# Optimization experiments

Measured on AMD Instinct MI355X. Metric: run time of the kernel, lower is better.

## Reference

```python
import jax, jax.numpy as jnp
import numpy as np

MULT = 20.0 / 2 ** (5 - 2)  # level=2, num_levels=5, div_flow=20 -> 2.5
PATCH = 7
PAD = PATCH // 2


def up_flow_fn(flow, w):
    # ConvTranspose2d(2, 2, 4, stride=2, padding=1, groups=2, bias=False)
    wf = w[:, :, ::-1, ::-1]  # flip kernel -> equivalent dilated conv
    return jax.lax.conv_general_dilated(
        flow, wf, window_strides=(1, 1), padding=((2, 2), (2, 2)),
        lhs_dilation=(2, 2), dimension_numbers=('NCHW', 'OIHW', 'NCHW'),
        feature_group_count=2)


def warp(x, flow, mult):
    # ptlflow LiteFlowNet WarpingLayer: normalized grid + flow/div_flow, grid_sample
    # (border padding, align_corners=True) masked by zero-padded ones-sample >= 1.
    B, C, H, W = x.shape
    gx = jnp.linspace(-1.0, 1.0, W, dtype=x.dtype)[None, None, :]
    gy = jnp.linspace(-1.0, 1.0, H, dtype=x.dtype)[None, :, None]
    sx = gx + flow[:, 0] * (2.0 * mult / max(W - 1, 1))
    sy = gy + flow[:, 1] * (2.0 * mult / max(H - 1, 1))
    px = (sx + 1.0) * 0.5 * (W - 1)  # unnormalized coords, align_corners=True
    py = (sy + 1.0) * 0.5 * (H - 1)
    # --- border-padded bilinear sample of x ---
    pxc = jnp.clip(px, 0.0, W - 1.0)
    pyc = jnp.clip(py, 0.0, H - 1.0)
    x0 = jnp.floor(pxc); y0 = jnp.floor(pyc)
    tx = pxc - x0; ty = pyc - y0
    x0i = x0.astype(jnp.int32); y0i = y0.astype(jnp.int32)
    x1i = jnp.minimum(x0i + 1, W - 1); y1i = jnp.minimum(y0i + 1, H - 1)
    img = jnp.transpose(x, (0, 2, 3, 1))  # BHWC for gathers
    b = jnp.arange(B)[:, None, None]
    v00 = img[b, y0i, x0i]; v01 = img[b, y0i, x1i]
    v10 = img[b, y1i, x0i]; v11 = img[b, y1i, x1i]
    out = (v00 * ((1 - tx) * (1 - ty))[..., None] + v01 * (tx * (1 - ty))[..., None]
           + v10 * ((1 - tx) * ty)[..., None] + v11 * (tx * ty)[..., None])
    # --- zero-padded bilinear sample of ones -> validity mask ---
    fx0 = jnp.floor(px); fy0 = jnp.floor(py)
    mtx = px - fx0; mty = py - fy0
    m = jnp.zeros_like(px)
    for dy, dx, wgt in ((0, 0, (1 - mtx) * (1 - mty)), (0, 1, mtx * (1 - mty)),
                        (1, 0, (1 - mtx) * mty), (1, 1, mtx * mty)):
        xi = fx0 + dx; yi = fy0 + dy
        inb = (xi >= 0) & (xi <= W - 1) & (yi >= 0) & (yi <= H - 1)
        m = m + wgt * inb.astype(x.dtype)
    mask = (m >= 1.0).astype(x.dtype)[..., None]
    return jnp.transpose(out * mask, (0, 3, 1, 2))


def correlation(f1, f2):
    # SpatialCorrelationSampler(kernel_size=1, patch_size=7, stride=1, dilation_patch=1)
    # corr[b,d,i,j] = sum_c f1[b,c,i,j] * f2[b,c,i+di-3,j+dj-3] (zero pad), d = 7*di+dj
    B, C, H, W = f1.shape
    f2p = jnp.pad(f2, ((0, 0), (0, 0), (PAD, PAD), (PAD, PAD)))
    outs = [jnp.sum(f1 * f2p[:, :, di:di + H, dj:dj + W], axis=1)
            for di in range(PATCH) for dj in range(PATCH)]
    return jnp.stack(outs, axis=1)  # [B, 49, H, W]


def conv2d(x, w, b, pad):
    y = jax.lax.conv_general_dilated(
        x, w, window_strides=(1, 1), padding=((pad, pad), (pad, pad)),
        dimension_numbers=('NCHW', 'OIHW', 'NCHW'))
    return y + b[None, :, None, None]


def setup_inputs() -> dict:
    key = jax.random.key(0)
    ks = jax.random.split(key, 11)
    B, C, H, W = 4, 128, 192, 320
    feats = jax.random.normal(ks[0], (B, 2, C, H, W), jnp.float32)
    flow = jax.random.normal(ks[1], (B, 2, H // 2, W // 2), jnp.float32)
    up_w = jax.random.normal(ks[2], (2, 1, 4, 4), jnp.float32) * 0.25
    w1 = jax.random.normal(ks[3], (128, 49, 3, 3), jnp.float32) * 0.05
    b1 = jnp.zeros((128,), jnp.float32)
    w2 = jax.random.normal(ks[4], (64, 128, 3, 3), jnp.float32) * 0.03
    b2 = jnp.zeros((64,), jnp.float32)
    w3 = jax.random.normal(ks[5], (32, 64, 3, 3), jnp.float32) * 0.04
    b3 = jnp.zeros((32,), jnp.float32)
    w4 = jax.random.normal(ks[6], (2, 32, 5, 5), jnp.float32) * 0.03
    b4 = jnp.zeros((2,), jnp.float32)
    return {"feats": feats, "flow": flow, "up_w": up_w, "w1": w1, "b1": b1,
            "w2": w2, "b2": b2, "w3": w3, "b3": b3, "w4": w4, "b4": b4}


def reference(feats, flow, up_w, w1, b1, w2, b2, w3, b3, w4, b4):
    C = feats.shape[2]
    flow_up = up_flow_fn(flow, up_w)                    # [B,2,H,W]
    warped2 = warp(feats[:, 1], flow_up, MULT)          # warp feat2 by flow*mult
    corr = correlation(feats[:, 0], warped2)            # [B,49,H,W]
    corr = jax.nn.leaky_relu(corr, 0.1) / C
    h = jax.nn.leaky_relu(conv2d(corr, w1, b1, 1), 0.1)
    h = jax.nn.leaky_relu(conv2d(h, w2, b2, 1), 0.1)
    h = jax.nn.leaky_relu(conv2d(h, w3, b3, 1), 0.1)
    new_flow = conv2d(h, w4, b4, 2)                     # flow_kernel_size=5, pad=2
    return flow_up + new_flow
```

## Files before the change

kernel.cpp:

```cpp
#include <hip/hip_runtime.h>

typedef __attribute__((ext_vector_type(8))) short short8;
typedef __attribute__((ext_vector_type(4))) float f32x4;
typedef __attribute__((ext_vector_type(16))) float f32x16;
typedef unsigned int uint;

constexpr int B = 4, C = 128, H = 192, W = 320;
constexpr int HW_ = H * W;

__device__ __forceinline__ unsigned short f2bf(float x) {
    uint u = __float_as_uint(x);
    u += 0x7fffu + ((u >> 16) & 1u);
    return (unsigned short)(u >> 16);
}
__device__ __forceinline__ uint pack2bf(float a, float b) {
    return (uint)f2bf(a) | ((uint)f2bf(b) << 16);
}

__global__ __launch_bounds__(256) void upflow_kernel(
    const float* __restrict__ flow, const float* __restrict__ up_w,
    double* __restrict__ flow_up)
{
#pragma clang fp contract(off)
    int idx = blockIdx.x * 256 + threadIdx.x;
    if (idx >= B * 2 * HW_) return;
    int x = idx % W;
    int y = (idx / W) % H;
    int c = (idx / HW_) % 2;
    int b = idx / (2 * HW_);
    double acc = 0.0;
    #pragma unroll
    for (int ky = 0; ky < 4; ++ky) {
        int p = y + ky - 2;
        if (p < 0 || (p & 1) || (p >> 1) >= 96) continue;
        #pragma unroll
        for (int kx = 0; kx < 4; ++kx) {
            int q = x + kx - 2;
            if (q < 0 || (q & 1) || (q >> 1) >= 160) continue;
            double fv = (double)flow[((b * 2 + c) * 96 + (p >> 1)) * 160 + (q >> 1)];
            double wv = (double)up_w[c * 16 + (3 - ky) * 4 + (3 - kx)];
            double prod = fv * wv;
            acc = acc + prod;
        }
    }
    flow_up[idx] = acc;
}

__global__ __launch_bounds__(256) void warp_kernel(
    const float* __restrict__ feats, const double* __restrict__ flow_up,
    uint* __restrict__ wp)
{
#pragma clang fp contract(off)
    int raw = blockIdx.x;
    int eb  = (raw & 7) * 240 + (raw >> 3);
    int g = eb / 960;
    int idx = (eb % 960) * 256 + threadIdx.x;
    int x = idx % W;
    int y = (idx / W) % H;
    int b = idx / HW_;

    double f0 = flow_up[(size_t)(b * 2 + 0) * HW_ + y * W + x];
    double f1 = flow_up[(size_t)(b * 2 + 1) * HW_ + y * W + x];

    double stepx = 2.0 / (double)(W - 1);
    double stepy = 2.0 / (double)(H - 1);
    double gx = (x == W - 1) ? 1.0 : ((double)x * stepx + (-1.0));
    double gy = (y == H - 1) ? 1.0 : ((double)y * stepy + (-1.0));
    double cxs = 2.0 * 2.5 / (double)(W - 1);
    double cys = 2.0 * 2.5 / (double)(H - 1);
    double sx = gx + f0 * cxs;
    double sy = gy + f1 * cys;
    double px = (sx + 1.0) * 0.5 * (double)(W - 1);
    double py = (sy + 1.0) * 0.5 * (double)(H - 1);

    double pxc = px < 0.0 ? 0.0 : (px > (double)(W - 1) ? (double)(W - 1) : px);
    double pyc = py < 0.0 ? 0.0 : (py > (double)(H - 1) ? (double)(H - 1) : py);
    double x0 = floor(pxc), y0 = floor(pyc);
    double tx = pxc - x0, ty = pyc - y0;
    int x0i = (int)x0, y0i = (int)y0;
    int y1i = min(y0i + 1, H - 1);

    double fx0 = floor(px), fy0 = floor(py);
    double mtx = px - fx0, mty = py - fy0;
    double w00 = (1.0 - mtx) * (1.0 - mty);
    double w01 = mtx * (1.0 - mty);
    double w10 = (1.0 - mtx) * mty;
    double w11 = mtx * mty;
    double m = 0.0;
    double xi, yi;
    xi = fx0;       yi = fy0;
    if (xi >= 0.0 && xi <= (double)(W - 1) && yi >= 0.0 && yi <= (double)(H - 1)) m = m + w00;
    xi = fx0 + 1.0; yi = fy0;
    if (xi >= 0.0 && xi <= (double)(W - 1) && yi >= 0.0 && yi <= (double)(H - 1)) m = m + w01;
    xi = fx0;       yi = fy0 + 1.0;
    if (xi >= 0.0 && xi <= (double)(W - 1) && yi >= 0.0 && yi <= (double)(H - 1)) m = m + w10;
    xi = fx0 + 1.0; yi = fy0 + 1.0;
    if (xi >= 0.0 && xi <= (double)(W - 1) && yi >= 0.0 && yi <= (double)(H - 1)) m = m + w11;
    float mask = (m >= 1.0) ? 1.0f : 0.0f;

    float a00 = (float)((1.0 - tx) * (1.0 - ty)) * mask;
    float a01 = (float)(tx * (1.0 - ty)) * mask;
    float a10 = (float)((1.0 - tx) * ty) * mask;
    float a11 = (float)(tx * ty) * mask;

    int base = min(x0i, W - 2);
    bool xe = (x0i == W - 1);
    int r0 = y0i * W + base;
    int r1 = y1i * W + base;

    const float* img = feats + (size_t)(b * 2 + 1) * C * HW_;
    uint* dst = wp + (size_t)b * 64 * HW_ + y * W + x;
    #pragma unroll 4
    for (int c2 = g * 32; c2 < g * 32 + 32; ++c2) {
        const float* p0 = img + (size_t)(2 * c2) * HW_;
        const float* p1 = p0 + HW_;
        float2 L0 = *(const float2*)&p0[r0];
        float2 L1 = *(const float2*)&p0[r1];
        float2 M0 = *(const float2*)&p1[r0];
        float2 M1 = *(const float2*)&p1[r1];
        float v00 = xe ? L0.y : L0.x;
        float v10 = xe ? L1.y : L1.x;
        float u00 = xe ? M0.y : M0.x;
        float u10 = xe ? M1.y : M1.x;
        float lo = a00 * v00 + a01 * L0.y + a10 * v10 + a11 * L1.y;
        float hi = a00 * u00 + a01 * M0.y + a10 * u10 + a11 * M1.y;
        dst[(size_t)c2 * HW_] = pack2bf(lo, hi);
    }
}

__global__ __launch_bounds__(256) void repack_w_kernel(
    const float* __restrict__ w1, const float* __restrict__ w2,
    const float* __restrict__ w3, const float* __restrict__ w4,
    unsigned short* __restrict__ wr)
{
    int idx = blockIdx.x * 256 + threadIdx.x;
    if (idx >= 178688) return;
    float v = 0.f;
    if (idx < 73728) {
        int tap = idx / 8192, r = idx % 8192, co = r / 64, ci = r % 64;
        if (ci < 49) v = w1[(co * 49 + ci) * 9 + tap];
    } else if (idx < 147456) {
        int i2 = idx - 73728;
        int tap = i2 / 8192, r = i2 % 8192, co = r / 128, ci = r % 128;
        v = w2[(co * 128 + ci) * 9 + tap];
    } else if (idx < 165888) {
        int i3 = idx - 147456;
        int tap = i3 / 2048, r = i3 % 2048, co = r / 64, ci = r % 64;
        v = w3[(co * 64 + ci) * 9 + tap];
    } else {
        int i4 = idx - 165888;
        int tap = i4 / 512, r = i4 % 512, co = r / 32, ci = r % 32;
        if (co < 2) v = w4[(co * 32 + ci) * 25 + tap];
    }
    wr[idx] = f2bf(v);
}

__global__ __launch_bounds__(256, 4) void corr_kernel(
    const float* __restrict__ feats, const uint* __restrict__ wp,
    uint* __restrict__ corrb)
{
    constexpr int SP = 42;
    __shared__ unsigned short lds[(320 + 64) * SP];
    float* stage = (float*)lds;

    int raw = blockIdx.x;
    int t = (raw & 7) * 480 + (raw >> 3);
    int xt = t % 10, yg = (t / 10) % 96, b = t / 960;
    int x0 = xt * 32, y0 = yg * 2;
    int tid = threadIdx.x;
    int lane = tid & 63, wave = tid >> 6;
    int lanelo = lane & 15, laneq = (lane >> 4) & 3;
    int h = wave & 1, yr = wave >> 1;

    int baddr[10], di_t[10], c_t[10];
    #pragma unroll
    for (int tt = 0; tt < 10; ++tt) {
        int p = tt * 16 + lanelo;
        int di = p / 22, cc = p - di * 22;
        di_t[tt] = di; c_t[tt] = cc;
        int addr = ((yr + di) * 40 + h * 16 + cc + 1) * SP + laneq * 8;
        baddr[tt] = (di > 6) ? 0 : addr;
    }
    int qaddr = (320 + yr * 32 + h * 16 + lanelo) * SP + laneq * 8;

    f32x4 acc[10];
    #pragma unroll
    for (int tt = 0; tt < 10; ++tt) acc[tt] = f32x4{0.f, 0.f, 0.f, 0.f};

    const uint* wpb = wp + (size_t)b * 64 * HW_;
    const float* f1b = feats + (size_t)(b * 2) * C * HW_;

    for (int ck = 0; ck < 4; ++ck) {
        if (ck) __syncthreads();
        #pragma unroll
        for (int i = 0; i < 5; ++i) {
            int u = tid + i * 256;
            int q = u % 10, pp = (u / 10) & 15, r = u / 160;
            int gy = y0 - 3 + r, gx0 = x0 - 4 + 4 * q;
            uint4 v = {0, 0, 0, 0};
            if (gy >= 0 && gy < H && gx0 >= 0 && gx0 < W)
                v = *(const uint4*)&wpb[(size_t)(ck * 16 + pp) * HW_ + gy * W + gx0];
            int pxb = (r * 40 + 4 * q) * SP + 2 * pp;
            *(uint*)&lds[pxb]          = v.x;
            *(uint*)&lds[pxb + SP]     = v.y;
            *(uint*)&lds[pxb + 2 * SP] = v.z;
            *(uint*)&lds[pxb + 3 * SP] = v.w;
        }
        #pragma unroll
        for (int i = 0; i < 4; ++i) {
            int u = tid + i * 256;
            int px = u & 63, pp = u >> 6;
            int gx = x0 + (px & 31), gy = y0 + (px >> 5);
            const float* p0 = f1b + (size_t)(ck * 32 + 2 * pp) * HW_ + gy * W + gx;
            *(uint*)&lds[(320 + px) * SP + 2 * pp] = pack2bf(p0[0], p0[HW_]);
        }
        __syncthreads();
        const short8 qf = *(const short8*)&lds[qaddr];
        #pragma unroll
        for (int tt = 0; tt < 10; ++tt) {
            const short8 kf = *(const short8*)&lds[baddr[tt]];
            acc[tt] = __builtin_amdgcn_mfma_f32_16x16x32_bf16(qf, kf, acc[tt], 0, 0, 0);
        }
    }
    __syncthreads();
    #pragma unroll
    for (int tt = 0; tt < 10; ++tt) {
        int di = di_t[tt];
        #pragma unroll
        for (int reg = 0; reg < 4; ++reg) {
            int i = laneq * 4 + reg;
            int dj = c_t[tt] - i;
            if (di <= 6 && dj >= 0 && dj < 7)
                stage[(di * 7 + dj) * 65 + yr * 32 + h * 16 + i] = acc[tt][reg];
        }
    }
    __syncthreads();
    uint* outp = corrb + (size_t)b * 32 * HW_;
    #pragma unroll
    for (int i = 0; i < 8; ++i) {
        int u = tid + i * 256;
        int px = u & 63, k2 = u >> 6;
        int gx = x0 + (px & 31), gy = y0 + (px >> 5);
        float v0 = (2 * k2 < 49) ? stage[(2 * k2) * 65 + px] : 0.f;
        float v1 = (2 * k2 + 1 < 49) ? stage[(2 * k2 + 1) * 65 + px] : 0.f;
        v0 = v0 > 0.f ? v0 : 0.1f * v0;
        v1 = v1 > 0.f ? v1 : 0.1f * v1;
        outp[(size_t)k2 * HW_ + gy * W + gx] = pack2bf(v0 * (1.f / 128.f), v1 * (1.f / 128.f));
    }
}

template<int CINP, int COUTP, int WCO, int WROWS, int MG, int NR, int MINW>
__global__ __launch_bounds__(256, MINW) void conv3x3_kernel(
    const uint* __restrict__ in, const unsigned short* __restrict__ wr,
    const float* __restrict__ bias, uint* __restrict__ outp, int cpx)
{
    constexpr int TH = WROWS * NR;
    constexpr int RH = TH + 2;
    constexpr int RW = 40, S2 = 21;
    constexpr int CHUNKS = CINP / 32;
    __shared__ uint lds32[RH * RW * S2];

    int tid = threadIdx.x;
    int lane = tid & 63, wave = tid >> 6;
    int lane5 = lane & 31, kg = lane >> 5;
    int cow = (WCO == 1) ? 0 : (wave & 1);
    int rowg = (WCO == 1) ? wave : (wave >> 1);

    int raw = blockIdx.x;
    int bx = (raw & 7) * cpx + (raw >> 3);
    int xt = bx % 10;
    int yt = (bx / 10) % (H / TH);
    int b = bx / (10 * (H / TH));
    int tx0 = xt * 32, ty0 = yt * TH;
    int cob = cow * MG * 32;

    f32x16 acc[MG][NR];
    #pragma unroll
    for (int mg = 0; mg < MG; ++mg)
        #pragma unroll
        for (int nr = 0; nr < NR; ++nr)
            #pragma unroll
            for (int j = 0; j < 16; ++j) acc[mg][nr][j] = 0.f;

    const uint* inb = in + (size_t)b * (CINP / 2) * HW_;

    for (int ck = 0; ck < CHUNKS; ++ck) {
        if (ck) __syncthreads();
        constexpr int UNITS = RH * 10 * 16;
        for (int s = tid; s < UNITS; s += 256) {
            int q = s % 10;
            int pp = (s / 10) % 16;
            int r = s / 160;
            int gy = ty0 - 1 + r;
            int gx0 = tx0 - 4 + 4 * q;
            uint4 v = {0, 0, 0, 0};
            if (gy >= 0 && gy < H && gx0 >= 0 && gx0 < W)
                v = *(const uint4*)&inb[(size_t)(ck * 16 + pp) * HW_ + gy * W + gx0];
            int pbase = (r * RW + 4 * q) * S2 + pp;
            lds32[pbase]          = v.x;
            lds32[pbase + S2]     = v.y;
            lds32[pbase + 2 * S2] = v.z;
            lds32[pbase + 3 * S2] = v.w;
        }
        __syncthreads();

        for (int tap = 0; tap < 9; ++tap) {
            int ky = tap / 3, kx = tap - ky * 3;
            short8 A[MG][2];
            #pragma unroll
            for (int mg = 0; mg < MG; ++mg)
                #pragma unroll
                for (int ks = 0; ks < 2; ++ks)
                    A[mg][ks] = *(const short8*)&wr[
                        ((size_t)tap * COUTP + cob + mg * 32 + lane5) * CINP +
                        ck * 32 + ks * 16 + kg * 8];
            #pragma unroll
            for (int nr = 0; nr < NR; ++nr) {
                int rr = rowg * NR + nr + ky;
                int col = lane5 + kx + 3;
                #pragma unroll
                for (int ks = 0; ks < 2; ++ks) {
                    const short8 Bf = *(const short8*)&lds32[(rr * RW + col) * S2 + ks * 8 + kg * 4];
                    #pragma unroll
                    for (int mg = 0; mg < MG; ++mg)
                        acc[mg][nr] = __builtin_amdgcn_mfma_f32_32x32x16_bf16(
                            A[mg][ks], Bf, acc[mg][nr], 0, 0, 0);
                }
            }
        }
    }

    int xg = tx0 + lane5;
    #pragma unroll
    for (int mg = 0; mg < MG; ++mg)
        #pragma unroll
        for (int nr = 0; nr < NR; ++nr) {
            int ygl = ty0 + rowg * NR + nr;
            #pragma unroll
            for (int j = 0; j < 8; ++j) {
                int com = ((2 * j) & 3) + 8 * (j >> 1) + 4 * kg;
                int co = cob + mg * 32 + com;
                float v0 = acc[mg][nr][2 * j] + bias[co];
                float v1 = acc[mg][nr][2 * j + 1] + bias[co + 1];
                v0 = v0 > 0.f ? v0 : 0.1f * v0;
                v1 = v1 > 0.f ? v1 : 0.1f * v1;
                outp[((size_t)b * (COUTP / 2) + (co >> 1)) * HW_ + ygl * W + xg] =
                    pack2bf(v0, v1);
            }
        }
}

template<int CINP, int COUTP, int M_TILES, int N_TILES, int KS, int MINW>
__global__ __launch_bounds__(256, MINW) void conv_mfma_kernel(
    const uint* __restrict__ in, const unsigned short* __restrict__ wr,
    const float* __restrict__ bias, float* __restrict__ outp,
    const double* __restrict__ flow_up, int coutReal, int cpx)
{
    constexpr int CHUNK = 32;
    constexpr int PADK = KS / 2;
    constexpr int PX_GROUPS = 4 / M_TILES;
    constexpr int TH = PX_GROUPS * (N_TILES / 2);
    constexpr int RH = TH + KS - 1;
    constexpr int RW = 40;
    constexpr int S2 = 21;
    constexpr int CHUNKS = CINP / CHUNK;
    __shared__ uint lds32[RH * RW * S2];

    int tid = threadIdx.x;
    int lanelo = tid & 15, laneq = (tid >> 4) & 3, wave = tid >> 6;
    int m_idx = wave % M_TILES, pgroup = wave / M_TILES;
    int pg_row0 = pgroup * (N_TILES / 2);

    int raw = blockIdx.x;
    int bx = (raw & 7) * cpx + (raw >> 3);
    int xt = bx % 10;
    int yt = (bx / 10) % (H / TH);
    int b = bx / (10 * (H / TH));
    int tx0 = xt * 32, ty0 = yt * TH;
    int cob = m_idx * 16;

    f32x4 acc[N_TILES];
    #pragma unroll
    for (int n = 0; n < N_TILES; ++n) acc[n] = f32x4{0.f, 0.f, 0.f, 0.f};

    const uint* inb = in + (size_t)b * (CINP / 2) * HW_;

    for (int ck = 0; ck < CHUNKS; ++ck) {
        constexpr int UNITS = RH * (CHUNK / 2) * 10;
        for (int s = tid; s < UNITS; s += 256) {
            int q = s % 10;
            int pp = (s / 10) % (CHUNK / 2);
            int r = s / (10 * (CHUNK / 2));
            int gy = ty0 - PADK + r;
            int gx0 = tx0 - 4 + q * 4;
            uint4 v = {0, 0, 0, 0};
            if (gy >= 0 && gy < H && gx0 >= 0 && gx0 < W)
                v = *(const uint4*)&inb[(size_t)(ck * (CHUNK / 2) + pp) * HW_ + gy * W + gx0];
            int pbase = (r * RW + q * 4) * S2 + pp;
            lds32[pbase] = v.x;
            lds32[pbase + S2] = v.y;
            lds32[pbase + 2 * S2] = v.z;
            lds32[pbase + 3 * S2] = v.w;
        }
        __syncthreads();

        short8 afr[KS * KS];
        #pragma unroll
        for (int tap = 0; tap < KS * KS; ++tap)
            afr[tap] = *(const short8*)&wr[
                ((size_t)tap * COUTP + cob + lanelo) * CINP + ck * CHUNK + laneq * 8];

        for (int tap = 0; tap < KS * KS; ++tap) {
            int ky = tap / KS, kx = tap - ky * KS;
            #pragma unroll
            for (int n = 0; n < N_TILES; ++n) {
                int rr = pg_row0 + (n >> 1) + ky;
                int pxi = (n & 1) * 16 + lanelo + (4 - PADK) + kx;
                const short8 bf = *(const short8*)&lds32[(rr * RW + pxi) * S2 + laneq * 4];
                acc[n] = __builtin_amdgcn_mfma_f32_16x16x32_bf16(afr[tap], bf, acc[n], 0, 0, 0);
            }
        }
        __syncthreads();
    }

    #pragma unroll
    for (int n = 0; n < N_TILES; ++n) {
        int x = tx0 + (n & 1) * 16 + lanelo;
        int y = ty0 + pg_row0 + (n >> 1);
        #pragma unroll
        for (int j = 0; j < 4; ++j) {
            int co = cob + laneq * 4 + j;
            if (co < coutReal) {
                float v = acc[n][j] + bias[co];
                v += (float)flow_up[((size_t)(b * 2) + co) * HW_ + y * W + x];
                outp[((size_t)b * coutReal + co) * HW_ + y * W + x] = v;
            }
        }
    }
}

extern "C" void kernel_launch(void* const* d_in, const int* in_sizes, int n_in,
                              void* d_out, int out_size, void* d_ws, size_t ws_size,
                              hipStream_t stream)
{
    const float* feats = (const float*)d_in[0];
    const float* flow  = (const float*)d_in[1];
    const float* up_w  = (const float*)d_in[2];
    const float* w1 = (const float*)d_in[3];
    const float* b1 = (const float*)d_in[4];
    const float* w2 = (const float*)d_in[5];
    const float* b2 = (const float*)d_in[6];
    const float* w3 = (const float*)d_in[7];
    const float* b3 = (const float*)d_in[8];
    const float* w4 = (const float*)d_in[9];
    const float* b4 = (const float*)d_in[10];
    float* out = (float*)d_out;

    char* ws = (char*)d_ws;
    double* flow_up = (double*)ws;
    uint* wp    = (uint*)(ws + 3932160);
    uint* h1    = (uint*)(ws + 3932160);
    uint* corrb = (uint*)(ws + 66846720);
    uint* h2    = corrb;
    uint* h3    = (uint*)(ws + 98304000);
    unsigned short* wr = (unsigned short*)(ws + 114032640);
    unsigned short* wr1 = wr;
    unsigned short* wr2 = wr + 73728;
    unsigned short* wr3 = wr + 147456;
    unsigned short* wr4 = wr + 165888;

    repack_w_kernel<<<699, 256, 0, stream>>>(w1, w2, w3, w4, wr);
    upflow_kernel<<<(B * 2 * HW_ + 255) / 256, 256, 0, stream>>>(flow, up_w, flow_up);
    warp_kernel<<<1920, 256, 0, stream>>>(feats, flow_up, wp);
    corr_kernel<<<3840, 256, 0, stream>>>(feats, wp, corrb);

    conv3x3_kernel<64, 128, 2, 2, 2, 2, 3>
        <<<1920, 256, 0, stream>>>(corrb, wr1, b1, h1, 240);
    conv3x3_kernel<128, 64, 1, 4, 2, 2, 3>
        <<<960, 256, 0, stream>>>(h1, wr2, b2, h2, 120);
    conv3x3_kernel<64, 32, 1, 4, 1, 2, 3>
        <<<960, 256, 0, stream>>>(h2, wr3, b3, h3, 120);
    conv_mfma_kernel<32, 16, 1, 2, 5, 2>
        <<<1920, 256, 0, stream>>>(h3, wr4, b4, out, flow_up, 2, 240);
}
```

Measured before the change: 705.1 us.

## Register-prefetch next input chunk during MFMA compute in correlation and conv3x3

Splits the per-chunk global-to-LDS staging in the correlation and 3x3 conv kernels into an issue phase (global loads into registers) and a commit phase (register-to-LDS stores). The loads for chunk ck+1 are issued right after the barrier, before the MFMA work on chunk ck, so their latency can hide behind compute. This removes the serialized load stall at the start of each chunk. In exchange it raises register pressure (up to NL uint4 per thread in conv, 5 uint4 plus 8 floats in correlation), which may lower occupancy under the existing launch bounds.

Result: slower. 765.0 us (+8.5%).

```diff
diff --git a/kernel.cpp b/kernel.cpp
--- a/kernel.cpp
+++ b/kernel.cpp
@@ -190,8 +190,10 @@
     const uint* wpb = wp + (size_t)b * 64 * HW_;
     const float* f1b = feats + (size_t)(b * 2) * C * HW_;
 
-    for (int ck = 0; ck < 4; ++ck) {
-        if (ck) __syncthreads();
+    uint4 pk[5];
+    float q0v[4], q1v[4];
+
+    auto issue = [&](int ck) {
         #pragma unroll
         for (int i = 0; i < 5; ++i) {
             int u = tid + i * 256;
@@ -200,11 +202,7 @@
             uint4 v = {0, 0, 0, 0};
             if (gy >= 0 && gy < H && gx0 >= 0 && gx0 < W)
                 v = *(const uint4*)&wpb[(size_t)(ck * 16 + pp) * HW_ + gy * W + gx0];
-            int pxb = (r * 40 + 4 * q) * SP + 2 * pp;
-            *(uint*)&lds[pxb]          = v.x;
-            *(uint*)&lds[pxb + SP]     = v.y;
-            *(uint*)&lds[pxb + 2 * SP] = v.z;
-            *(uint*)&lds[pxb + 3 * SP] = v.w;
+            pk[i] = v;
         }
         #pragma unroll
         for (int i = 0; i < 4; ++i) {
@@ -212,17 +210,42 @@
             int px = u & 63, pp = u >> 6;
             int gx = x0 + (px & 31), gy = y0 + (px >> 5);
             const float* p0 = f1b + (size_t)(ck * 32 + 2 * pp) * HW_ + gy * W + gx;
-            *(uint*)&lds[(320 + px) * SP + 2 * pp] = pack2bf(p0[0], p0[HW_]);
-        }
+            q0v[i] = p0[0];
+            q1v[i] = p0[HW_];
+        }
+    };
+    auto commit = [&]() {
+        #pragma unroll
+        for (int i = 0; i < 5; ++i) {
+            int u = tid + i * 256;
+            int q = u % 10, pp = (u / 10) & 15, r = u / 160;
+            int pxb = (r * 40 + 4 * q) * SP + 2 * pp;
+            *(uint*)&lds[pxb]          = pk[i].x;
+            *(uint*)&lds[pxb + SP]     = pk[i].y;
+            *(uint*)&lds[pxb + 2 * SP] = pk[i].z;
+            *(uint*)&lds[pxb + 3 * SP] = pk[i].w;
+        }
+        #pragma unroll
+        for (int i = 0; i < 4; ++i) {
+            int u = tid + i * 256;
+            int px = u & 63, pp = u >> 6;
+            *(uint*)&lds[(320 + px) * SP + 2 * pp] = pack2bf(q0v[i], q1v[i]);
+        }
+    };
+
+    issue(0);
+    for (int ck = 0; ck < 4; ++ck) {
+        commit();
         __syncthreads();
+        if (ck < 3) issue(ck + 1);
         const short8 qf = *(const short8*)&lds[qaddr];
         #pragma unroll
         for (int tt = 0; tt < 10; ++tt) {
             const short8 kf = *(const short8*)&lds[baddr[tt]];
             acc[tt] = __builtin_amdgcn_mfma_f32_16x16x32_bf16(qf, kf, acc[tt], 0, 0, 0);
         }
-    }
-    __syncthreads();
+        __syncthreads();
+    }
     #pragma unroll
     for (int tt = 0; tt < 10; ++tt) {
         int di = di_t[tt];
@@ -258,6 +281,8 @@
     constexpr int RH = TH + 2;
     constexpr int RW = 40, S2 = 21;
     constexpr int CHUNKS = CINP / 32;
+    constexpr int UNITS = RH * 10 * 16;
+    constexpr int NL = (UNITS + 255) / 256;
     __shared__ uint lds32[RH * RW * S2];
 
     int tid = threadIdx.x;
@@ -284,25 +309,46 @@
 
     const uint* inb = in + (size_t)b * (CINP / 2) * HW_;
 
+    uint4 pre[NL];
+    auto issue = [&](int ck) {
+        #pragma unroll
+        for (int i = 0; i < NL; ++i) {
+            int s = tid + i * 256;
+            uint4 v = {0, 0, 0, 0};
+            if (s < UNITS) {
+                int q = s % 10;
+                int pp = (s / 10) % 16;
+                int r = s / 160;
+                int gy = ty0 - 1 + r;
+                int gx0 = tx0 - 4 + 4 * q;
+                if (gy >= 0 && gy < H && gx0 >= 0 && gx0 < W)
+                    v = *(const uint4*)&inb[(size_t)(ck * 16 + pp) * HW_ + gy * W + gx0];
+            }
+            pre[i] = v;
+        }
+    };
+    auto commit = [&]() {
+        #pragma unroll
+        for (int i = 0; i < NL; ++i) {
+            int s = tid + i * 256;
+            if (s < UNITS) {
+                int q = s % 10;
+                int pp = (s / 10) % 16;
+                int r = s / 160;
+                int pbase = (r * RW + 4 * q) * S2 + pp;
+                lds32[pbase]          = pre[i].x;
+                lds32[pbase + S2]     = pre[i].y;
+                lds32[pbase + 2 * S2] = pre[i].z;
+                lds32[pbase + 3 * S2] = pre[i].w;
+            }
+        }
+    };
+
+    issue(0);
     for (int ck = 0; ck < CHUNKS; ++ck) {
-        if (ck) __syncthreads();
-        constexpr int UNITS = RH * 10 * 16;
-        for (int s = tid; s < UNITS; s += 256) {
-            int q = s % 10;
-            int pp = (s / 10) % 16;
-            int r = s / 160;
-            int gy = ty0 - 1 + r;
-            int gx0 = tx0 - 4 + 4 * q;
-            uint4 v = {0, 0, 0, 0};
-            if (gy >= 0 && gy < H && gx0 >= 0 && gx0 < W)
-                v = *(const uint4*)&inb[(size_t)(ck * 16 + pp) * HW_ + gy * W + gx0];
-            int pbase = (r * RW + 4 * q) * S2 + pp;
-            lds32[pbase]          = v.x;
-            lds32[pbase + S2]     = v.y;
-            lds32[pbase + 2 * S2] = v.z;
-            lds32[pbase + 3 * S2] = v.w;
-        }
+        commit();
         __syncthreads();
+        if (ck + 1 < CHUNKS) issue(ck + 1);
 
         for (int tap = 0; tap < 9; ++tap) {
             int ky = tap / 3, kx = tap - ky * 3;
@@ -328,6 +374,7 @@
                 }
             }
         }
+        if (ck + 1 < CHUNKS) __syncthreads();
     }
 
     int xg = tx0 + lane5;
```
